# Kernel tuning notes

Hardware: AMD Instinct MI355X
Metric: run time of the kernel (lower is better)

## Reference

```python
import jax, jax.numpy as jnp
import numpy as np

HIDDEN = 1024
B, S = 64, 512
EPS = 1e-10


def setup_inputs() -> dict:
    key = jax.random.key(0)
    k1, k2, k3, k4, k5 = jax.random.split(key, 5)
    encoder_outputs = jax.random.normal(k1, (B, S, HIDDEN), dtype=jnp.float32)
    decoder_hidden = jax.random.normal(k2, (B, HIDDEN), dtype=jnp.float32)
    inp_mask = (jax.random.uniform(k3, (S, B)) > 0.2).astype(jnp.float32)
    # W_h: Linear(2H -> H, bias=False); torch stores weight as (out, in)
    W_h = jax.random.normal(k4, (HIDDEN, 2 * HIDDEN), dtype=jnp.float32) / np.sqrt(2 * HIDDEN)
    stdv = 1.0 / np.sqrt(HIDDEN)
    v = jax.random.normal(k5, (HIDDEN,), dtype=jnp.float32) * stdv
    return {"encoder_outputs": encoder_outputs, "decoder_hidden": decoder_hidden,
            "inp_mask": inp_mask, "W_h": W_h, "v": v}


def reference(encoder_outputs, decoder_hidden, inp_mask, W_h, v):
    # encoder_outputs: [B, S, H]; decoder_hidden: [B, H]; inp_mask: [S, B]
    seq_len = encoder_outputs.shape[1]
    # H = decoder_hidden broadcast over seq: [B, S, H] (avoid explicit repeat)
    Hrep = jnp.broadcast_to(decoder_hidden[:, None, :], encoder_outputs.shape)
    cat = jnp.concatenate([Hrep, encoder_outputs], axis=2)          # [B, S, 2H]
    energy = jnp.tanh(jnp.einsum('bsk,hk->bsh', cat, W_h))          # [B, S, H]
    scores = jnp.einsum('bsh,h->bs', energy, v)                     # [B, S]
    # NOTE: original applies softmax over dim=0 (the batch dim) — faithful here
    a = jax.nn.softmax(scores, axis=0) * inp_mask.T                 # [B, S]
    a = a / (jnp.sum(a, axis=1, keepdims=True) + EPS)
    context = jnp.einsum('bs,bsh->bh', a, encoder_outputs)[:, None, :]  # [B, 1, H]
    return a[:, None, :], context
```

## Files before the change

### kernel.cpp

```cpp
#include <hip/hip_runtime.h>

#define B_ 64
#define S_ 512
#define H_ 1024
#define M_ (B_*S_)

typedef unsigned int u32;
typedef unsigned short u16;
typedef __attribute__((ext_vector_type(8))) short bf16x8;
typedef __attribute__((ext_vector_type(4))) float f32x4;

__device__ __forceinline__ u16 f2bf(float f) {
  u32 u = __builtin_bit_cast(u32, f);
  u += 0x7fffu + ((u >> 16) & 1u);
  return (u16)(u >> 16);
}
__device__ __forceinline__ u32 pk2(float a, float b) {
  return (u32)f2bf(a) | ((u32)f2bf(b) << 16);
}
__device__ __forceinline__ float tanh_fast(float x) {
  x = fminf(fmaxf(x, -20.f), 20.f);
  float e = __expf(2.f * x);
  return (e - 1.f) / (e + 1.f);
}
__device__ __forceinline__ void gload_lds16(const u16* g, u16* l) {
  __builtin_amdgcn_global_load_lds(
      (const __attribute__((address_space(1))) u32*)g,
      (__attribute__((address_space(3))) u32*)l, 16, 0, 0);
}

__global__ void conv_w2(const float* __restrict__ Wh, u16* __restrict__ W2bf) {
  int idx = blockIdx.x * 256 + threadIdx.x;
  int n = idx >> 8;
  int k = (idx & 255) * 4;
  float4 x = *(const float4*)(Wh + (size_t)n * 2048 + 1024 + k);
  uint2 p; p.x = pk2(x.x, x.y); p.y = pk2(x.z, x.w);
  *(uint2*)(W2bf + (size_t)n * 1024 + k) = p;
}

__global__ void part1_kernel(const float* __restrict__ dh,
                             const float* __restrict__ Wh,
                             float* __restrict__ part1) {
  __shared__ float dhs[1024];
  int t = threadIdx.x;
  int hc = blockIdx.x;
  int b  = blockIdx.y;
  ((float4*)dhs)[t] = ((const float4*)(dh + b * 1024))[t];
  __syncthreads();
  int h = hc * 256 + t;
  const float4* wr = (const float4*)(Wh + (size_t)h * 2048);
  const float4* dv = (const float4*)dhs;
  float acc = 0.f;
#pragma unroll 8
  for (int k4 = 0; k4 < 256; ++k4) {
    float4 w = wr[k4];
    float4 d = dv[k4];
    acc += w.x * d.x + w.y * d.y + w.z * d.z + w.w * d.w;
  }
  part1[b * 1024 + h] = acc;
}

__global__ __launch_bounds__(256) void gemm_scores(
    const float* __restrict__ enc, const u16* __restrict__ W2bf,
    const float* __restrict__ part1, const float* __restrict__ v,
    float* __restrict__ scores) {
  __shared__ __align__(16) u16 As[128 * 64];
  __shared__ __align__(16) u16 Bs[128 * 64];
  __shared__ float sc_lds[128];
  const int tid = threadIdx.x;
  const int lane = tid & 63, wid = tid >> 6;
  const int wr = wid >> 1, wc = wid & 1;
  const int l15 = lane & 15, lhi = lane >> 4;
  const int r0 = blockIdx.x * 128;
  const int n0 = blockIdx.y * 128;
  const int bb = r0 >> 9;

  f32x4 acc[4][4] = {};

  const int brow = wid * 8 + (lane >> 3);
  const int bk = (lane & 7) * 8;

  for (int k0 = 0; k0 < 1024; k0 += 64) {
#pragma unroll
    for (int c = 0; c < 4; ++c) {
      const u16* src = W2bf + (size_t)(n0 + c * 32 + brow) * 1024 + k0 + bk;
      gload_lds16(src, Bs + c * 2048 + wid * 512);
    }
#pragma unroll
    for (int i = 0; i < 4; ++i) {
      int f = 2 * tid + 512 * i;
      int arow = f >> 4, c4 = f & 15;
      const float4* src =
          (const float4*)(enc + (size_t)(r0 + arow) * 1024 + k0 + c4 * 4);
      float4 x = src[0], y = src[1];
      uint4 p;
      p.x = pk2(x.x, x.y); p.y = pk2(x.z, x.w);
      p.z = pk2(y.x, y.y); p.w = pk2(y.z, y.w);
      *(uint4*)&As[arow * 64 + c4 * 4] = p;
    }
    __syncthreads();
#pragma unroll
    for (int kk = 0; kk < 2; ++kk) {
      const int kofs = kk * 32 + lhi * 8;
      bf16x8 af[4], bfr[4];
#pragma unroll
      for (int i = 0; i < 4; ++i)
        af[i] = *(const bf16x8*)&As[(wr * 64 + i * 16 + l15) * 64 + kofs];
#pragma unroll
      for (int j = 0; j < 4; ++j)
        bfr[j] = *(const bf16x8*)&Bs[(wc * 64 + j * 16 + l15) * 64 + kofs];
#pragma unroll
      for (int i = 0; i < 4; ++i)
#pragma unroll
        for (int j = 0; j < 4; ++j)
          acc[i][j] = __builtin_amdgcn_mfma_f32_16x16x32_bf16(
              af[i], bfr[j], acc[i][j], 0, 0, 0);
    }
    __syncthreads();
  }

  if (tid < 128) sc_lds[tid] = 0.f;
  __syncthreads();
  float ps[4][4] = {};
#pragma unroll
  for (int j = 0; j < 4; ++j) {
    int col = n0 + wc * 64 + j * 16 + l15;
    float pv = part1[bb * 1024 + col];
    float vv = v[col];
#pragma unroll
    for (int i = 0; i < 4; ++i)
#pragma unroll
      for (int q = 0; q < 4; ++q)
        ps[i][q] += tanh_fast(acc[i][j][q] + pv) * vv;
  }
#pragma unroll
  for (int i = 0; i < 4; ++i)
#pragma unroll
    for (int q = 0; q < 4; ++q)
      atomicAdd(&sc_lds[wr * 64 + i * 16 + lhi * 4 + q], ps[i][q]);
  __syncthreads();
  if (tid < 128) atomicAdd(&scores[r0 + tid], sc_lds[tid]);
}

__global__ void softmax_col(const float* __restrict__ scores,
                            const float* __restrict__ mask,
                            float* __restrict__ a_raw) {
  int s = blockIdx.x;
  int b = threadIdx.x;
  float x = scores[b * 512 + s];
  float m = x;
  for (int o = 32; o; o >>= 1) m = fmaxf(m, __shfl_xor(m, o));
  float e = __expf(x - m);
  float sum = e;
  for (int o = 32; o; o >>= 1) sum += __shfl_xor(sum, o);
  a_raw[b * 512 + s] = (e / sum) * mask[s * 64 + b];
}

__global__ void norm_rows(const float* __restrict__ a_raw,
                          float* __restrict__ out_a) {
  __shared__ float wsum[4];
  int b = blockIdx.x, t = threadIdx.x;
  float va = a_raw[b * 512 + t];
  float vb = a_raw[b * 512 + 256 + t];
  float sum = va + vb;
  for (int o = 32; o; o >>= 1) sum += __shfl_xor(sum, o);
  if ((t & 63) == 0) wsum[t >> 6] = sum;
  __syncthreads();
  float tot = wsum[0] + wsum[1] + wsum[2] + wsum[3];
  float inv = 1.f / (tot + 1e-10f);
  out_a[b * 512 + t] = va * inv;
  out_a[b * 512 + 256 + t] = vb * inv;
}

__global__ void context_kernel(const float* __restrict__ a,
                               const float* __restrict__ enc,
                               float* __restrict__ ctx) {
  int b = blockIdx.x, hc = blockIdx.y, t = threadIdx.x;
  int h = hc * 128 + t;
  const float* ep = enc + (size_t)b * 512 * 1024 + h;
  const float* ap = a + b * 512;
  float acc = 0.f;
#pragma unroll 8
  for (int s = 0; s < 512; ++s) acc += ap[s] * ep[(size_t)s * 1024];
  ctx[b * 1024 + h] = acc;
}

extern "C" void kernel_launch(void* const* d_in, const int* in_sizes, int n_in,
                              void* d_out, int out_size, void* d_ws,
                              size_t ws_size, hipStream_t stream) {
  const float* enc  = (const float*)d_in[0];
  const float* dh   = (const float*)d_in[1];
  const float* mask = (const float*)d_in[2];
  const float* Wh   = (const float*)d_in[3];
  const float* v    = (const float*)d_in[4];
  float* out_a   = (float*)d_out;
  float* out_ctx = out_a + M_;

  char* ws = (char*)d_ws;
  u16*   W2bf   = (u16*)ws;
  float* part1  = (float*)(ws + (2u << 20));
  float* scores = (float*)(ws + (2u << 20) + (256u << 10));
  float* a_raw  = (float*)(ws + (2u << 20) + (384u << 10));

  hipMemsetAsync(scores, 0, M_ * sizeof(float), stream);
  conv_w2<<<1024, 256, 0, stream>>>(Wh, W2bf);
  part1_kernel<<<dim3(4, 64), 256, 0, stream>>>(dh, Wh, part1);
  gemm_scores<<<dim3(256, 8), 256, 0, stream>>>(enc, W2bf, part1, v, scores);
  softmax_col<<<512, 64, 0, stream>>>(scores, mask, a_raw);
  norm_rows<<<64, 256, 0, stream>>>(a_raw, out_a);
  context_kernel<<<dim3(64, 8), 128, 0, stream>>>(out_a, enc, out_ctx);
}
```

Before: 455.9 us.

## Double-buffer GEMM with swizzled LDS, retile part1 and split context over sequence

The scores GEMM now double-buffers its A and B tiles in LDS. It prefetches the next K-slice into registers while the MFMAs run, applies an XOR swizzle to avoid bank conflicts, swaps the grid axes so blocks sharing an encoder tile run together, and sets occupancy to 2 blocks per CU. part1 becomes a tiled GEMM that accumulates over K chunks with atomics. The context kernel splits the sequence into 8 chunks and accumulates with atomics, which gives far more parallelism. These changes add memsets and make the float accumulation order nondeterministic.

```diff
diff --git a/kernel.cpp b/kernel.cpp
--- a/kernel.cpp
+++ b/kernel.cpp
@@ -41,74 +41,111 @@
 __global__ void part1_kernel(const float* __restrict__ dh,
                              const float* __restrict__ Wh,
                              float* __restrict__ part1) {
-  __shared__ float dhs[1024];
+  __shared__ float whs[16][132];
+  __shared__ float dhs[64][132];
   int t = threadIdx.x;
-  int hc = blockIdx.x;
-  int b  = blockIdx.y;
-  ((float4*)dhs)[t] = ((const float4*)(dh + b * 1024))[t];
-  __syncthreads();
-  int h = hc * 256 + t;
-  const float4* wr = (const float4*)(Wh + (size_t)h * 2048);
-  const float4* dv = (const float4*)dhs;
-  float acc = 0.f;
-#pragma unroll 8
-  for (int k4 = 0; k4 < 256; ++k4) {
-    float4 w = wr[k4];
-    float4 d = dv[k4];
-    acc += w.x * d.x + w.y * d.y + w.z * d.z + w.w * d.w;
-  }
-  part1[b * 1024 + h] = acc;
-}
-
-__global__ __launch_bounds__(256) void gemm_scores(
+  int h0 = blockIdx.x * 16;
+  int k0 = blockIdx.y * 128;
+#pragma unroll
+  for (int i = 0; i < 2; ++i) {
+    int idx = t + 256 * i;
+    int r = idx >> 5, c4 = idx & 31;
+    float4 x = *(const float4*)(Wh + (size_t)(h0 + r) * 2048 + k0 + c4 * 4);
+    *(float4*)&whs[r][c4 * 4] = x;
+  }
+#pragma unroll
+  for (int i = 0; i < 8; ++i) {
+    int idx = t + 256 * i;
+    int r = idx >> 5, c4 = idx & 31;
+    float4 x = *(const float4*)(dh + (size_t)r * 1024 + k0 + c4 * 4);
+    *(float4*)&dhs[r][c4 * 4] = x;
+  }
+  __syncthreads();
+  int b = t >> 2, hg = t & 3;
+  float acc[4] = {0.f, 0.f, 0.f, 0.f};
+#pragma unroll 4
+  for (int k = 0; k < 128; ++k) {
+    float d = dhs[b][k];
+#pragma unroll
+    for (int j = 0; j < 4; ++j) acc[j] += whs[hg * 4 + j][k] * d;
+  }
+#pragma unroll
+  for (int j = 0; j < 4; ++j)
+    atomicAdd(&part1[b * 1024 + h0 + hg * 4 + j], acc[j]);
+}
+
+__global__ __launch_bounds__(256, 2) void gemm_scores(
     const float* __restrict__ enc, const u16* __restrict__ W2bf,
     const float* __restrict__ part1, const float* __restrict__ v,
     float* __restrict__ scores) {
-  __shared__ __align__(16) u16 As[128 * 64];
-  __shared__ __align__(16) u16 Bs[128 * 64];
+  __shared__ __align__(16) u16 As[2][128 * 64];
+  __shared__ __align__(16) u16 Bs[2][128 * 64];
   __shared__ float sc_lds[128];
   const int tid = threadIdx.x;
   const int lane = tid & 63, wid = tid >> 6;
   const int wr = wid >> 1, wc = wid & 1;
   const int l15 = lane & 15, lhi = lane >> 4;
-  const int r0 = blockIdx.x * 128;
-  const int n0 = blockIdx.y * 128;
+  const int n0 = blockIdx.x * 128;
+  const int r0 = blockIdx.y * 128;
   const int bb = r0 >> 9;
 
   f32x4 acc[4][4] = {};
 
-  const int brow = wid * 8 + (lane >> 3);
-  const int bk = (lane & 7) * 8;
-
-  for (int k0 = 0; k0 < 1024; k0 += 64) {
+  const int brow8 = lane >> 3;
+  const int bks = ((lane & 7) ^ brow8) * 8;
+
+  {
 #pragma unroll
     for (int c = 0; c < 4; ++c) {
-      const u16* src = W2bf + (size_t)(n0 + c * 32 + brow) * 1024 + k0 + bk;
-      gload_lds16(src, Bs + c * 2048 + wid * 512);
+      const u16* src = W2bf + (size_t)(n0 + c * 32 + wid * 8 + brow8) * 1024 + bks;
+      gload_lds16(src, &Bs[0][c * 2048 + wid * 512]);
     }
 #pragma unroll
     for (int i = 0; i < 4; ++i) {
       int f = 2 * tid + 512 * i;
       int arow = f >> 4, c4 = f & 15;
-      const float4* src =
-          (const float4*)(enc + (size_t)(r0 + arow) * 1024 + k0 + c4 * 4);
-      float4 x = src[0], y = src[1];
-      uint4 p;
-      p.x = pk2(x.x, x.y); p.y = pk2(x.z, x.w);
+      const float4* srcA = (const float4*)(enc + (size_t)(r0 + arow) * 1024 + c4 * 4);
+      float4 x = srcA[0], y = srcA[1];
+      uint4 p; p.x = pk2(x.x, x.y); p.y = pk2(x.z, x.w);
       p.z = pk2(y.x, y.y); p.w = pk2(y.z, y.w);
-      *(uint4*)&As[arow * 64 + c4 * 4] = p;
+      *(uint4*)&As[0][arow * 64 + ((c4 * 4) ^ ((arow & 7) << 3))] = p;
     }
     __syncthreads();
+  }
+
+  int p = 0;
+  for (int t = 0; t < 16; ++t) {
+    float4 xa[4], ya[4];
+    if (t < 15) {
+      const int kn = (t + 1) * 64;
+#pragma unroll
+      for (int c = 0; c < 4; ++c) {
+        const u16* src =
+            W2bf + (size_t)(n0 + c * 32 + wid * 8 + brow8) * 1024 + kn + bks;
+        gload_lds16(src, &Bs[p ^ 1][c * 2048 + wid * 512]);
+      }
+#pragma unroll
+      for (int i = 0; i < 4; ++i) {
+        int f = 2 * tid + 512 * i;
+        int arow = f >> 4, c4 = f & 15;
+        const float4* srcA =
+            (const float4*)(enc + (size_t)(r0 + arow) * 1024 + kn + c4 * 4);
+        xa[i] = srcA[0]; ya[i] = srcA[1];
+      }
+    }
 #pragma unroll
     for (int kk = 0; kk < 2; ++kk) {
-      const int kofs = kk * 32 + lhi * 8;
       bf16x8 af[4], bfr[4];
 #pragma unroll
-      for (int i = 0; i < 4; ++i)
-        af[i] = *(const bf16x8*)&As[(wr * 64 + i * 16 + l15) * 64 + kofs];
-#pragma unroll
-      for (int j = 0; j < 4; ++j)
-        bfr[j] = *(const bf16x8*)&Bs[(wc * 64 + j * 16 + l15) * 64 + kofs];
+      for (int i = 0; i < 4; ++i) {
+        int ar = wr * 64 + i * 16 + l15;
+        af[i] = *(const bf16x8*)&As[p][ar * 64 + ((kk * 32 + lhi * 8) ^ ((ar & 7) << 3))];
+      }
+#pragma unroll
+      for (int j = 0; j < 4; ++j) {
+        int br = wc * 64 + j * 16 + l15;
+        bfr[j] = *(const bf16x8*)&Bs[p][br * 64 + ((kk * 32 + lhi * 8) ^ ((br & 7) << 3))];
+      }
 #pragma unroll
       for (int i = 0; i < 4; ++i)
 #pragma unroll
@@ -116,7 +153,19 @@
           acc[i][j] = __builtin_amdgcn_mfma_f32_16x16x32_bf16(
               af[i], bfr[j], acc[i][j], 0, 0, 0);
     }
-    __syncthreads();
+    if (t < 15) {
+#pragma unroll
+      for (int i = 0; i < 4; ++i) {
+        int f = 2 * tid + 512 * i;
+        int arow = f >> 4, c4 = f & 15;
+        uint4 pw;
+        pw.x = pk2(xa[i].x, xa[i].y); pw.y = pk2(xa[i].z, xa[i].w);
+        pw.z = pk2(ya[i].x, ya[i].y); pw.w = pk2(ya[i].z, ya[i].w);
+        *(uint4*)&As[p ^ 1][arow * 64 + ((c4 * 4) ^ ((arow & 7) << 3))] = pw;
+      }
+      __syncthreads();
+      p ^= 1;
+    }
   }
 
   if (tid < 128) sc_lds[tid] = 0.f;
@@ -175,14 +224,14 @@
 __global__ void context_kernel(const float* __restrict__ a,
                                const float* __restrict__ enc,
                                float* __restrict__ ctx) {
-  int b = blockIdx.x, hc = blockIdx.y, t = threadIdx.x;
-  int h = hc * 128 + t;
-  const float* ep = enc + (size_t)b * 512 * 1024 + h;
-  const float* ap = a + b * 512;
+  int b = blockIdx.x, hc = blockIdx.y, sc = blockIdx.z, t = threadIdx.x;
+  int h = hc * 256 + t;
+  const float* ep = enc + (size_t)b * 512 * 1024 + (size_t)sc * 64 * 1024 + h;
+  const float* ap = a + b * 512 + sc * 64;
   float acc = 0.f;
 #pragma unroll 8
-  for (int s = 0; s < 512; ++s) acc += ap[s] * ep[(size_t)s * 1024];
-  ctx[b * 1024 + h] = acc;
+  for (int s = 0; s < 64; ++s) acc += ap[s] * ep[(size_t)s * 1024];
+  atomicAdd(&ctx[b * 1024 + h], acc);
 }
 
 extern "C" void kernel_launch(void* const* d_in, const int* in_sizes, int n_in,
@@ -203,10 +252,12 @@
   float* a_raw  = (float*)(ws + (2u << 20) + (384u << 10));
 
   hipMemsetAsync(scores, 0, M_ * sizeof(float), stream);
+  hipMemsetAsync(part1, 0, B_ * H_ * sizeof(float), stream);
+  hipMemsetAsync(out_ctx, 0, B_ * H_ * sizeof(float), stream);
   conv_w2<<<1024, 256, 0, stream>>>(Wh, W2bf);
-  part1_kernel<<<dim3(4, 64), 256, 0, stream>>>(dh, Wh, part1);
-  gemm_scores<<<dim3(256, 8), 256, 0, stream>>>(enc, W2bf, part1, v, scores);
+  part1_kernel<<<dim3(64, 8), 256, 0, stream>>>(dh, Wh, part1);
+  gemm_scores<<<dim3(8, 256), 256, 0, stream>>>(enc, W2bf, part1, v, scores);
   softmax_col<<<512, 64, 0, stream>>>(scores, mask, a_raw);
   norm_rows<<<64, 256, 0, stream>>>(a_raw, out_a);
-  context_kernel<<<dim3(64, 8), 128, 0, stream>>>(out_a, enc, out_ctx);
-}
+  context_kernel<<<dim3(64, 4, 8), 256, 0, stream>>>(out_a, enc, out_ctx);
+}
```

Result: faster. 446.0 us (-2.2%).
